# Optimization experiments

Hardware: AMD Instinct MI355X
Metric: run time of the kernel (lower is better)

The kernel has to match this reference:

```python
import jax, jax.numpy as jnp
import numpy as np

N = 512
D = 512
# static upper-triangle pair indices (i < j)
_II, _JJ = np.triu_indices(N, k=1)
_II = jnp.asarray(_II)
_JJ = jnp.asarray(_JJ)


def setup_inputs() -> dict:
    key = jax.random.key(0)
    ks = jax.random.split(key, 9)
    s = 0.02
    return {
        'features': jax.random.normal(ks[0], (N, D), dtype=jnp.float32),
        # relation_classifier: Linear(2D->D), Linear(D->10)
        'cw1': jax.random.normal(ks[1], (2 * D, D), dtype=jnp.float32) * s,
        'cb1': jnp.zeros((D,), dtype=jnp.float32),
        'cw2': jax.random.normal(ks[2], (D, 10), dtype=jnp.float32) * s,
        'cb2': jnp.zeros((10,), dtype=jnp.float32),
        # relation_strength_calc: Linear(2D->D//2), Linear(D//2->1)
        'sw1': jax.random.normal(ks[3], (2 * D, D // 2), dtype=jnp.float32) * s,
        'sb1': jnp.zeros((D // 2,), dtype=jnp.float32),
        'sw2': jax.random.normal(ks[4], (D // 2, 1), dtype=jnp.float32) * s,
        'sb2': jnp.zeros((1,), dtype=jnp.float32),
    }


def reference(features, cw1, cb1, cw2, cb2, sw1, sb1, sw2, sb2):
    # cat([f_i, f_j]) @ W == f_i @ W[:D] + f_j @ W[D:]  (linear-split trick)
    # precompute per-node projections once, then gather per pair
    c_a = features @ cw1[:D]   # [N, D]
    c_b = features @ cw1[D:]   # [N, D]
    s_a = features @ sw1[:D]   # [N, D//2]
    s_b = features @ sw1[D:]   # [N, D//2]

    # classifier path
    h = jax.nn.relu(c_a[_II] + c_b[_JJ] + cb1)          # [P, D]
    relation_types = jax.nn.log_softmax(h @ cw2 + cb2)   # [P, 10]
    most_likely_relations = jnp.argmax(relation_types, axis=-1)  # [P]

    # strength path
    hs = jax.nn.relu(s_a[_II] + s_b[_JJ] + sb1)          # [P, D//2]
    relation_strengths = jax.nn.sigmoid(hs @ sw2 + sb2)   # [P, 1]

    return relation_types, most_likely_relations, relation_strengths
```

## Files before the change

kernel.cpp:

```cpp
#include <hip/hip_runtime.h>
#include <math.h>

#define NN 512
#define DD 512
#define NPAIRS 130816
#define TYPES_OFF 0
#define ARGMAX_OFF 1308160
#define STRENGTH_OFF 1438976


__device__ __forceinline__ void fma64_step(
    const float4& a0, const float4& a1,
    const float4& b0, const float4& b1, const float4& b2, const float4& b3,
    double acc[2][4])
{
    const float av[2][4] = {{a0.x,a0.y,a0.z,a0.w},{a1.x,a1.y,a1.z,a1.w}};
    const float bv[4][4] = {{b0.x,b0.y,b0.z,b0.w},{b1.x,b1.y,b1.z,b1.w},
                            {b2.x,b2.y,b2.z,b2.w},{b3.x,b3.y,b3.z,b3.w}};
    #pragma unroll
    for (int kk = 0; kk < 4; ++kk) {
        double ad0 = (double)av[0][kk], ad1 = (double)av[1][kk];
        #pragma unroll
        for (int c = 0; c < 4; ++c) {
            double bd = (double)bv[kk][c];
            acc[0][c] = fma(ad0, bd, acc[0][c]);
            acc[1][c] = fma(ad1, bd, acc[1][c]);
        }
    }
}

__device__ __forceinline__ void fma32_step(
    const float4& a0, const float4& a1,
    const float4& b0, const float4& b1, const float4& b2, const float4& b3,
    float acc[2][4])
{
    const float av[2][4] = {{a0.x,a0.y,a0.z,a0.w},{a1.x,a1.y,a1.z,a1.w}};
    const float bv[4][4] = {{b0.x,b0.y,b0.z,b0.w},{b1.x,b1.y,b1.z,b1.w},
                            {b2.x,b2.y,b2.z,b2.w},{b3.x,b3.y,b3.z,b3.w}};
    #pragma unroll
    for (int kk = 0; kk < 4; ++kk) {
        #pragma unroll
        for (int c = 0; c < 4; ++c) {
            acc[0][c] = fmaf(av[0][kk], bv[kk][c], acc[0][c]);
            acc[1][c] = fmaf(av[1][kk], bv[kk][c], acc[1][c]);
        }
    }
}

__global__ __launch_bounds__(256, 4) void proj_kernel(
    const float* __restrict__ F, const float* __restrict__ cw1,
    const float* __restrict__ sw1,
    const float* __restrict__ cb1, const float* __restrict__ sb1,
    const float* __restrict__ cw2,
    double* __restrict__ ca0, double* __restrict__ ca1,
    double* __restrict__ cb0, double* __restrict__ cbp1,
    float* __restrict__ sa0, float* __restrict__ sa1,
    float* __restrict__ sb0, float* __restrict__ sbp1,
    double* __restrict__ cw2d)
{
    const int t = threadIdx.x;
    if (blockIdx.x >= 768) {
        int idx = (blockIdx.x - 768) * 256 + t;
        if (idx < 5120) cw2d[idx] = (double)cw2[idx];
        return;
    }
    const int wid  = blockIdx.x * 4 + (t >> 6);
    const int lane = t & 63;
    const int mg = lane >> 4;
    const int nq = lane & 15;

    if (wid < 2048) {
        const int z  = wid & 1;
        const int r  = wid >> 1;
        const int nt = r & 15;
        const int mt = r >> 4;
        const int m0 = mt * 8;
        const int n  = nt * 64;
        const float* W = (n < 512) ? cw1 : cw1 + 512 * 512;
        const int n0   = (n < 512) ? n : n - 512;
        double* outp   = (n < 512) ? (z ? ca1 : ca0) : (z ? cbp1 : cb0);
        const bool addbias = (z == 0) && (n < 512);

        const int row0 = m0 + mg * 2;
        const int col0 = n0 + nq * 4;
        const float* pa0 = F + row0 * 512 + z * 256;
        const float* pa1 = pa0 + 512;
        const float* pb  = W + (z * 256) * 512 + col0;

        double acc[2][4];
        #pragma unroll
        for (int rr = 0; rr < 2; ++rr)
            #pragma unroll
            for (int cc = 0; cc < 4; ++cc) acc[rr][cc] = 0.0;

        float4 a0 = *(const float4*)(pa0);
        float4 a1 = *(const float4*)(pa1);
        float4 b0 = *(const float4*)(pb);
        float4 b1 = *(const float4*)(pb + 512);
        float4 b2 = *(const float4*)(pb + 1024);
        float4 b3 = *(const float4*)(pb + 1536);
        for (int s = 0; s < 63; ++s) {
            float4 na0 = *(const float4*)(pa0 + (s + 1) * 4);
            float4 na1 = *(const float4*)(pa1 + (s + 1) * 4);
            const float* nb = pb + (s + 1) * 2048;
            float4 nb0 = *(const float4*)(nb);
            float4 nb1 = *(const float4*)(nb + 512);
            float4 nb2 = *(const float4*)(nb + 1024);
            float4 nb3 = *(const float4*)(nb + 1536);
            fma64_step(a0, a1, b0, b1, b2, b3, acc);
            a0 = na0; a1 = na1; b0 = nb0; b1 = nb1; b2 = nb2; b3 = nb3;
        }
        fma64_step(a0, a1, b0, b1, b2, b3, acc);

        #pragma unroll
        for (int rr = 0; rr < 2; ++rr) {
            double v[4];
            #pragma unroll
            for (int cc = 0; cc < 4; ++cc) {
                v[cc] = acc[rr][cc];
                if (addbias) v[cc] += (double)cb1[col0 + cc];
            }
            double* dst = outp + (row0 + rr) * 512 + col0;
            *(double2*)(dst + 0) = make_double2(v[0], v[1]);
            *(double2*)(dst + 2) = make_double2(v[2], v[3]);
        }
    } else {
        const int w2 = wid - 2048;
        const int z  = w2 & 1;
        const int r  = w2 >> 1;
        const int nt = r & 7;
        const int mt = r >> 3;
        const int m0 = mt * 8;
        const int n  = nt * 64;
        const float* W = (n < 256) ? sw1 : sw1 + 512 * 256;
        const int n0   = (n < 256) ? n : n - 256;
        float* outp    = (n < 256) ? (z ? sa1 : sa0) : (z ? sbp1 : sb0);
        const bool addbias = (z == 0) && (n < 256);

        const int row0 = m0 + mg * 2;
        const int col0 = n0 + nq * 4;
        const float* pa0 = F + row0 * 512 + z * 256;
        const float* pa1 = pa0 + 512;
        const float* pb  = W + (z * 256) * 256 + col0;

        float acc[2][4];
        #pragma unroll
        for (int rr = 0; rr < 2; ++rr)
            #pragma unroll
            for (int cc = 0; cc < 4; ++cc) acc[rr][cc] = 0.f;

        float4 a0 = *(const float4*)(pa0);
        float4 a1 = *(const float4*)(pa1);
        float4 b0 = *(const float4*)(pb);
        float4 b1 = *(const float4*)(pb + 256);
        float4 b2 = *(const float4*)(pb + 512);
        float4 b3 = *(const float4*)(pb + 768);
        for (int s = 0; s < 63; ++s) {
            float4 na0 = *(const float4*)(pa0 + (s + 1) * 4);
            float4 na1 = *(const float4*)(pa1 + (s + 1) * 4);
            const float* nb = pb + (s + 1) * 1024;
            float4 nb0 = *(const float4*)(nb);
            float4 nb1 = *(const float4*)(nb + 256);
            float4 nb2 = *(const float4*)(nb + 512);
            float4 nb3 = *(const float4*)(nb + 768);
            fma32_step(a0, a1, b0, b1, b2, b3, acc);
            a0 = na0; a1 = na1; b0 = nb0; b1 = nb1; b2 = nb2; b3 = nb3;
        }
        fma32_step(a0, a1, b0, b1, b2, b3, acc);

        #pragma unroll
        for (int rr = 0; rr < 2; ++rr) {
            float4 v = make_float4(acc[rr][0], acc[rr][1], acc[rr][2], acc[rr][3]);
            if (addbias) {
                v.x += sb1[col0 + 0]; v.y += sb1[col0 + 1];
                v.z += sb1[col0 + 2]; v.w += sb1[col0 + 3];
            }
            *(float4*)(outp + (row0 + rr) * 256 + col0) = v;
        }
    }
}

__global__ __launch_bounds__(256, 4) void pair_kernel(
    const double* __restrict__ ca0, const double* __restrict__ ca1,
    const double* __restrict__ cb0, const double* __restrict__ cbp1,
    const float* __restrict__ sa0, const float* __restrict__ sa1,
    const float* __restrict__ sb0, const float* __restrict__ sbp1,
    const double* __restrict__ cw2d, const float* __restrict__ cb2,
    const float* __restrict__ sw2, const float* __restrict__ sb2,
    float* __restrict__ out)
{
    const int b = blockIdx.x;
    int bi = (int)floorf((129.0f - sqrtf(16641.0f - 8.0f * (float)b)) * 0.5f);
    while ((bi + 1) * (129 - (bi + 1)) / 2 <= b) ++bi;
    while (bi * (129 - bi) / 2 > b) --bi;
    const int bj = bi + (b - bi * (129 - bi) / 2);
    const int i0 = bi * 8, j0 = bj * 8;

    const int t = threadIdx.x;
    const int q  = t >> 6;
    const int qu = __builtin_amdgcn_readfirstlane(q);
    const int l = t & 63;
    const int pi = l >> 3, pj = l & 7;
    const int i = i0 + pi, j = j0 + pj;

    __shared__ double smem_d[2176];
    double* sA  = smem_d;
    double* sB  = smem_d + 1088;
    float*  sSa = (float*)smem_d;
    float*  sSb = (float*)smem_d + 2176;
    double* lgbuf = smem_d;
    float*  stbuf = (float*)(smem_d + 1920);

    #pragma unroll
    for (int u = 0; u < 4; ++u) {
        int idx = u * 256 + t;
        int kq  = idx & 15;
        int row = (idx >> 4) & 7;
        int qq  = (idx >> 7) & 3;
        int arr = idx >> 9;
        int off = (arr ? (j0 + row) : (i0 + row)) * 256 + qq * 64 + kq * 4;
        const float* s0 = arr ? sb0 : sa0;
        const float* s1 = arr ? sbp1 : sa1;
        float4 v0 = *(const float4*)(s0 + off);
        float4 v1 = *(const float4*)(s1 + off);
        float4 v = make_float4(v0.x + v1.x, v0.y + v1.y, v0.z + v1.z, v0.w + v1.w);
        float* dst = (arr ? sSb : sSa) + (qq * 8 + row) * 68 + kq * 4;
        *(float4*)dst = v;
    }
    __syncthreads();
    float accs = 0.f;
    {
        const float* sw2q = sw2 + qu * 64;
        const float* ra = sSa + (q * 8 + pi) * 68;
        const float* rb = sSb + (q * 8 + pj) * 68;
        #pragma unroll 16
        for (int kk = 0; kk < 64; ++kk) {
            float h = fmaxf(ra[kk] + rb[kk], 0.f);
            accs = fmaf(h, sw2q[kk], accs);
        }
    }

    double lg[10];
    #pragma unroll
    for (int c = 0; c < 10; ++c) lg[c] = 0.0;
    const double* wq = cw2d + qu * 1280;

    for (int c4 = 0; c4 < 4; ++c4) {
        __syncthreads();
        #pragma unroll
        for (int u = 0; u < 4; ++u) {
            int idx = u * 256 + t;
            int kq  = idx & 15;
            int row = (idx >> 4) & 7;
            int qq  = (idx >> 7) & 3;
            int arr = idx >> 9;
            int off = (arr ? (j0 + row) : (i0 + row)) * 512 + qq * 128 + c4 * 32 + kq * 2;
            const double* d0 = arr ? cb0 : ca0;
            const double* d1 = arr ? cbp1 : ca1;
            double2 u0 = *(const double2*)(d0 + off);
            double2 u1 = *(const double2*)(d1 + off);
            double2 v = make_double2(u0.x + u1.x, u0.y + u1.y);
            double* dst = (arr ? sB : sA) + (qq * 8 + row) * 34 + kq * 2;
            *(double2*)dst = v;
        }
        __syncthreads();
        const double* ra = sA + (q * 8 + pi) * 34;
        const double* rb = sB + (q * 8 + pj) * 34;
        const double* wc = wq + c4 * 320;
        #pragma unroll 8
        for (int kk = 0; kk < 32; ++kk) {
            double h = fmax(ra[kk] + rb[kk], 0.0);
            const double* w = wc + kk * 10;
            #pragma unroll
            for (int c = 0; c < 10; ++c) lg[c] = fma(h, w[c], lg[c]);
        }
    }

    __syncthreads();
    if (q > 0) {
        double* dst = lgbuf + ((q - 1) * 64 + l) * 10;
        #pragma unroll
        for (int c = 0; c < 10; ++c) dst[c] = lg[c];
        stbuf[(q - 1) * 64 + l] = accs;
    }
    __syncthreads();
    if (q == 0) {
        #pragma unroll
        for (int w = 0; w < 3; ++w) {
            const double* srcb = lgbuf + (w * 64 + l) * 10;
            #pragma unroll
            for (int c = 0; c < 10; ++c) lg[c] += srcb[c];
        }
        float st = accs + stbuf[l] + stbuf[64 + l] + stbuf[128 + l] + sb2[0];

        #pragma unroll
        for (int c = 0; c < 10; ++c) lg[c] += (double)cb2[c];
        double mx = lg[0]; int am2 = 0;
        #pragma unroll
        for (int c = 1; c < 10; ++c) {
            if (lg[c] > mx) { mx = lg[c]; am2 = c; }
        }
        float tf[10]; float s = 0.f;
        #pragma unroll
        for (int c = 0; c < 10; ++c) { tf[c] = (float)(lg[c] - mx); s += __expf(tf[c]); }
        float ls = __logf(s);

        if (j > i) {
            const int p = i * 511 - (i * (i - 1)) / 2 + (j - i - 1);
            float* tp = out + TYPES_OFF + p * 10;
            #pragma unroll
            for (int c = 0; c < 10; ++c) tp[c] = tf[c] - ls;
            out[ARGMAX_OFF + p] = (float)am2;
            out[STRENGTH_OFF + p] = 1.0f / (1.0f + __expf(-st));
        }
    }
}

extern "C" void kernel_launch(void* const* d_in, const int* in_sizes, int n_in,
                              void* d_out, int out_size, void* d_ws, size_t ws_size,
                              hipStream_t stream) {
    const float* F   = (const float*)d_in[0];
    const float* cw1 = (const float*)d_in[1];
    const float* cb1 = (const float*)d_in[2];
    const float* cw2 = (const float*)d_in[3];
    const float* cb2 = (const float*)d_in[4];
    const float* sw1 = (const float*)d_in[5];
    const float* sb1 = (const float*)d_in[6];
    const float* sw2 = (const float*)d_in[7];
    const float* sb2 = (const float*)d_in[8];
    float* out = (float*)d_out;

    char* ws = (char*)d_ws;
    double* ca0  = (double*)(ws);
    double* ca1  = (double*)(ws + 2097152);
    double* cb0  = (double*)(ws + 4194304);
    double* cbp1 = (double*)(ws + 6291456);
    float*  sa0  = (float*)(ws + 8388608);
    float*  sa1  = (float*)(ws + 8912896);
    float*  sb0  = (float*)(ws + 9437184);
    float*  sbp1 = (float*)(ws + 9961472);
    double* cw2d = (double*)(ws + 10485760);

    hipLaunchKernelGGL(proj_kernel, dim3(788), dim3(256), 0, stream,
                       F, cw1, sw1, cb1, sb1, cw2,
                       ca0, ca1, cb0, cbp1, sa0, sa1, sb0, sbp1, cw2d);
    hipLaunchKernelGGL(pair_kernel, dim3(2080), dim3(256), 0, stream,
                       ca0, ca1, cb0, cbp1, sa0, sa1, sb0, sbp1,
                       cw2d, cb2, sw2, sb2, out);
}
```

Measured before the change: 151.9 us.

## Compute pair logits in fp32 with fp64 argmax recheck on near-ties

The classifier second layer in the pair kernel now accumulates in fp32 (shared tiles and weights in float) instead of fp64, which is much cheaper on the vector units. Pairs whose top-two logits differ by less than a small threshold are recomputed in fp64 by the whole wavefront to keep the argmax exact. The separate cw2-to-double conversion blocks are removed from the projection kernel. The risk is that the fixed gap threshold may not cover all fp32 rounding cases, and divergent fallback loops add cost when many near-ties occur.

```diff
diff --git a/kernel.cpp b/kernel.cpp
--- a/kernel.cpp
+++ b/kernel.cpp
@@ -7,6 +7,8 @@
 #define TYPES_OFF 0
 #define ARGMAX_OFF 1308160
 #define STRENGTH_OFF 1438976
+
+#define GAP_THRESH 2.5e-4f
 
 
 __device__ __forceinline__ void fma64_step(
@@ -51,19 +53,12 @@
     const float* __restrict__ F, const float* __restrict__ cw1,
     const float* __restrict__ sw1,
     const float* __restrict__ cb1, const float* __restrict__ sb1,
-    const float* __restrict__ cw2,
     double* __restrict__ ca0, double* __restrict__ ca1,
     double* __restrict__ cb0, double* __restrict__ cbp1,
     float* __restrict__ sa0, float* __restrict__ sa1,
-    float* __restrict__ sb0, float* __restrict__ sbp1,
-    double* __restrict__ cw2d)
+    float* __restrict__ sb0, float* __restrict__ sbp1)
 {
     const int t = threadIdx.x;
-    if (blockIdx.x >= 768) {
-        int idx = (blockIdx.x - 768) * 256 + t;
-        if (idx < 5120) cw2d[idx] = (double)cw2[idx];
-        return;
-    }
     const int wid  = blockIdx.x * 4 + (t >> 6);
     const int lane = t & 63;
     const int mg = lane >> 4;
@@ -185,7 +180,7 @@
     const double* __restrict__ cb0, const double* __restrict__ cbp1,
     const float* __restrict__ sa0, const float* __restrict__ sa1,
     const float* __restrict__ sb0, const float* __restrict__ sbp1,
-    const double* __restrict__ cw2d, const float* __restrict__ cb2,
+    const float* __restrict__ cw2, const float* __restrict__ cb2,
     const float* __restrict__ sw2, const float* __restrict__ sb2,
     float* __restrict__ out)
 {
@@ -203,13 +198,13 @@
     const int pi = l >> 3, pj = l & 7;
     const int i = i0 + pi, j = j0 + pj;
 
-    __shared__ double smem_d[2176];
-    double* sA  = smem_d;
-    double* sB  = smem_d + 1088;
-    float*  sSa = (float*)smem_d;
-    float*  sSb = (float*)smem_d + 2176;
-    double* lgbuf = smem_d;
-    float*  stbuf = (float*)(smem_d + 1920);
+    __shared__ __align__(16) float smem[4352];
+    float* sSa = smem;
+    float* sSb = smem + 2176;
+    float* sA  = smem;
+    float* sB  = smem + 2176;
+    float* lgbuf = smem;
+    float* stbuf = smem + 1920;
 
     #pragma unroll
     for (int u = 0; u < 4; ++u) {
@@ -240,12 +235,11 @@
         }
     }
 
-    double lg[10];
+    float lg[10];
     #pragma unroll
-    for (int c = 0; c < 10; ++c) lg[c] = 0.0;
-    const double* wq = cw2d + qu * 1280;
-
-    for (int c4 = 0; c4 < 4; ++c4) {
+    for (int c = 0; c < 10; ++c) lg[c] = 0.f;
+
+    for (int rnd = 0; rnd < 2; ++rnd) {
         __syncthreads();
         #pragma unroll
         for (int u = 0; u < 4; ++u) {
@@ -254,31 +248,34 @@
             int row = (idx >> 4) & 7;
             int qq  = (idx >> 7) & 3;
             int arr = idx >> 9;
-            int off = (arr ? (j0 + row) : (i0 + row)) * 512 + qq * 128 + c4 * 32 + kq * 2;
+            int off = (arr ? (j0 + row) : (i0 + row)) * 512 + qq * 128 + rnd * 64 + kq * 4;
             const double* d0 = arr ? cb0 : ca0;
             const double* d1 = arr ? cbp1 : ca1;
-            double2 u0 = *(const double2*)(d0 + off);
-            double2 u1 = *(const double2*)(d1 + off);
-            double2 v = make_double2(u0.x + u1.x, u0.y + u1.y);
-            double* dst = (arr ? sB : sA) + (qq * 8 + row) * 34 + kq * 2;
-            *(double2*)dst = v;
+            double2 x0 = *(const double2*)(d0 + off);
+            double2 x1 = *(const double2*)(d0 + off + 2);
+            double2 y0 = *(const double2*)(d1 + off);
+            double2 y1 = *(const double2*)(d1 + off + 2);
+            float4 v = make_float4((float)(x0.x + y0.x), (float)(x0.y + y0.y),
+                                   (float)(x1.x + y1.x), (float)(x1.y + y1.y));
+            float* dst = (arr ? sB : sA) + (qq * 8 + row) * 68 + kq * 4;
+            *(float4*)dst = v;
         }
         __syncthreads();
-        const double* ra = sA + (q * 8 + pi) * 34;
-        const double* rb = sB + (q * 8 + pj) * 34;
-        const double* wc = wq + c4 * 320;
+        const float* ra = sA + (q * 8 + pi) * 68;
+        const float* rb = sB + (q * 8 + pj) * 68;
+        const float* wr = cw2 + (qu * 128 + rnd * 64) * 10;
         #pragma unroll 8
-        for (int kk = 0; kk < 32; ++kk) {
-            double h = fmax(ra[kk] + rb[kk], 0.0);
-            const double* w = wc + kk * 10;
-            #pragma unroll
-            for (int c = 0; c < 10; ++c) lg[c] = fma(h, w[c], lg[c]);
+        for (int kk = 0; kk < 64; ++kk) {
+            float h = fmaxf(ra[kk] + rb[kk], 0.f);
+            const float* w = wr + kk * 10;
+            #pragma unroll
+            for (int c = 0; c < 10; ++c) lg[c] = fmaf(h, w[c], lg[c]);
         }
     }
 
     __syncthreads();
     if (q > 0) {
-        double* dst = lgbuf + ((q - 1) * 64 + l) * 10;
+        float* dst = lgbuf + ((q - 1) * 64 + l) * 10;
         #pragma unroll
         for (int c = 0; c < 10; ++c) dst[c] = lg[c];
         stbuf[(q - 1) * 64 + l] = accs;
@@ -287,23 +284,57 @@
     if (q == 0) {
         #pragma unroll
         for (int w = 0; w < 3; ++w) {
-            const double* srcb = lgbuf + (w * 64 + l) * 10;
+            const float* srcb = lgbuf + (w * 64 + l) * 10;
             #pragma unroll
             for (int c = 0; c < 10; ++c) lg[c] += srcb[c];
         }
         float st = accs + stbuf[l] + stbuf[64 + l] + stbuf[128 + l] + sb2[0];
 
         #pragma unroll
-        for (int c = 0; c < 10; ++c) lg[c] += (double)cb2[c];
-        double mx = lg[0]; int am2 = 0;
+        for (int c = 0; c < 10; ++c) lg[c] += cb2[c];
+
+        float mx = lg[0], mx2 = -3.0e38f; int am2 = 0;
         #pragma unroll
         for (int c = 1; c < 10; ++c) {
-            if (lg[c] > mx) { mx = lg[c]; am2 = c; }
-        }
-        float tf[10]; float s = 0.f;
-        #pragma unroll
-        for (int c = 0; c < 10; ++c) { tf[c] = (float)(lg[c] - mx); s += __expf(tf[c]); }
-        float ls = __logf(s);
+            if (lg[c] > mx) { mx2 = mx; mx = lg[c]; am2 = c; }
+            else if (lg[c] > mx2) mx2 = lg[c];
+        }
+
+        unsigned long long m = __ballot((j > i) && (mx - mx2 < GAP_THRESH));
+        while (m) {
+            const int s = __ffsll((unsigned long long)m) - 1; m &= (m - 1);
+            const int si = i0 + (s >> 3), sj = j0 + (s & 7);
+            double part[10];
+            #pragma unroll
+            for (int c = 0; c < 10; ++c) part[c] = 0.0;
+            const int kb = l * 8;
+            #pragma unroll 2
+            for (int kk = 0; kk < 8; ++kk) {
+                const int k = kb + kk;
+                double h = fmax(ca0[si * 512 + k] + ca1[si * 512 + k]
+                              + cb0[sj * 512 + k] + cbp1[sj * 512 + k], 0.0);
+                const float* w = cw2 + k * 10;
+                #pragma unroll
+                for (int c = 0; c < 10; ++c) part[c] = fma(h, (double)w[c], part[c]);
+            }
+            #pragma unroll
+            for (int off = 32; off > 0; off >>= 1) {
+                #pragma unroll
+                for (int c = 0; c < 10; ++c) part[c] += __shfl_xor(part[c], off, 64);
+            }
+            double bmx = part[0] + (double)cb2[0]; int ba = 0;
+            #pragma unroll
+            for (int c = 1; c < 10; ++c) {
+                double v = part[c] + (double)cb2[c];
+                if (v > bmx) { bmx = v; ba = c; }
+            }
+            if (l == s) am2 = ba;
+        }
+
+        float tf[10]; float ssum = 0.f;
+        #pragma unroll
+        for (int c = 0; c < 10; ++c) { tf[c] = lg[c] - mx; ssum += __expf(tf[c]); }
+        float ls = __logf(ssum);
 
         if (j > i) {
             const int p = i * 511 - (i * (i - 1)) / 2 + (j - i - 1);
@@ -339,12 +370,11 @@
     float*  sa1  = (float*)(ws + 8912896);
     float*  sb0  = (float*)(ws + 9437184);
     float*  sbp1 = (float*)(ws + 9961472);
-    double* cw2d = (double*)(ws + 10485760);
-
-    hipLaunchKernelGGL(proj_kernel, dim3(788), dim3(256), 0, stream,
-                       F, cw1, sw1, cb1, sb1, cw2,
-                       ca0, ca1, cb0, cbp1, sa0, sa1, sb0, sbp1, cw2d);
+
+    hipLaunchKernelGGL(proj_kernel, dim3(768), dim3(256), 0, stream,
+                       F, cw1, sw1, cb1, sb1,
+                       ca0, ca1, cb0, cbp1, sa0, sa1, sb0, sbp1);
     hipLaunchKernelGGL(pair_kernel, dim3(2080), dim3(256), 0, stream,
                        ca0, ca1, cb0, cbp1, sa0, sa1, sb0, sbp1,
-                       cw2d, cb2, sw2, sb2, out);
-}
+                       cw2, cb2, sw2, sb2, out);
+}
```

Result: faster. 146.1 us (-3.8%).
